# Kernel tuning notes

Hardware: AMD Instinct MI355X
Metric: run time of the kernel (lower is better)

Reference implementation:

```python
import jax, jax.numpy as jnp
import numpy as np

BANDWIDTH = 0.1
NUM_ITERS = 5


def setup_inputs() -> dict:
    key = jax.random.key(0)
    # image batch in [0,1], BCHW
    x = jax.random.uniform(key, (2, 3, 96, 96), dtype=jnp.float32)
    return {"x": x}


def reference(x):
    # Mean-shift filtering: each pixel feature y is iteratively moved to the
    # Gaussian-kernel weighted mean of ALL original pixel features:
    #   y_{t+1} = sum_j exp(-||y_t - x_j||^2 / (2 bw^2)) x_j / sum_j exp(...)
    B, C, H, W = x.shape
    N = H * W
    pts = x.reshape(B, C, N).transpose(0, 2, 1)  # [B, N, C] original points
    inv2bw2 = jnp.float32(1.0 / (2.0 * BANDWIDTH * BANDWIDTH))
    x_sq = jnp.sum(pts * pts, axis=-1)  # [B, N]

    def step(y, _):
        # squared pairwise distances via ||y||^2 + ||x||^2 - 2 y.x  -> [B, N, N]
        y_sq = jnp.sum(y * y, axis=-1)  # [B, N]
        d2 = y_sq[:, :, None] + x_sq[:, None, :] - 2.0 * jnp.einsum(
            'bnc,bmc->bnm', y, pts)
        w = jnp.exp(-jnp.maximum(d2, 0.0) * inv2bw2)  # Gaussian kernel weights
        num = jnp.einsum('bnm,bmc->bnc', w, pts)  # weighted sum of points
        den = jnp.sum(w, axis=-1, keepdims=True)  # normalizer (>= 1, self-weight)
        return num / den, None

    y, _ = jax.lax.scan(step, pts, None, length=NUM_ITERS)
    return y.transpose(0, 2, 1).reshape(B, C, H, W)
```

## Files before the change

### kernel.cpp

```cpp
#include <hip/hip_runtime.h>
#include <math.h>


#define NPTS 9216
#define NB 2
#define TOT (NB * NPTS)
#define NTIL 288
#define MSPL 6
#define MBLK 1536
#define TPW 12
#define LOG2E 1.44269504088896340736f

typedef float v2f __attribute__((ext_vector_type(2)));
typedef short bf16x8 __attribute__((ext_vector_type(8)));
typedef float f32x16 __attribute__((ext_vector_type(16)));

__device__ __forceinline__ unsigned short bf16r(float x) {
    unsigned u = __float_as_uint(x);
    return (unsigned short)((u + 0x7fffu + ((u >> 16) & 1u)) >> 16);
}
__device__ __forceinline__ float bf16f(unsigned short h) {
    return __uint_as_float((unsigned)h << 16);
}

__global__ __launch_bounds__(256) void ms_feat(const float* __restrict__ x,
                                               short* __restrict__ pfeat,
                                               float4* __restrict__ pts4,
                                               float s) {
    int gid = blockIdx.x * 256 + threadIdx.x;
    int b = gid / NPTS, m = gid - b * NPTS;
    const float* xb = x + b * 3 * NPTS;
    float p0 = xb[m] * s, p1 = xb[NPTS + m] * s, p2 = xb[2 * NPTS + m] * s;
    float np = -fmaf(p0, p0, fmaf(p1, p1, p2 * p2));
    float a0 = 2.f * p0, a1 = 2.f * p1, a2 = 2.f * p2;
    unsigned short Ah0 = bf16r(a0), Ah1 = bf16r(a1), Ah2 = bf16r(a2);
    unsigned short Al0 = bf16r(a0 - bf16f(Ah0));
    unsigned short Al1 = bf16r(a1 - bf16f(Ah1));
    unsigned short Al2 = bf16r(a2 - bf16f(Ah2));
    unsigned short Nh = bf16r(np);
    unsigned short Nl = bf16r(np - bf16f(Nh));
    uint4* dst = (uint4*)(pfeat + (size_t)gid * 16);
    dst[0] = make_uint4((unsigned)Ah0 | ((unsigned)Ah1 << 16),
                        (unsigned)Ah2 | ((unsigned)Ah0 << 16),
                        (unsigned)Ah1 | ((unsigned)Ah2 << 16),
                        (unsigned)Al0 | ((unsigned)Al1 << 16));
    dst[1] = make_uint4((unsigned)Al2 | ((unsigned)Al0 << 16),
                        (unsigned)Al1 | ((unsigned)Al2 << 16),
                        (unsigned)Nh  | ((unsigned)Nl  << 16), 0u);
    pts4[gid] = make_float4(p0, p1, p2, 1.0f);
}

__global__ __launch_bounds__(256, 4) void ms_iter(
    const float* __restrict__ x, const float4* __restrict__ accIn,
    float4* __restrict__ accOut, const short* __restrict__ pfeat,
    const float4* __restrict__ pts4, float s, int first) {

    __shared__ float4 lds4[MBLK];

    const int tid = threadIdx.x;
    const int l   = tid & 63;
    const int wv  = tid >> 6;
    const int col = l & 31;
    const int hi  = l >> 5;

    int bid = blockIdx.x;
    const int b  = bid / (MSPL * NTIL);
    int r        = bid - b * (MSPL * NTIL);
    const int nt = r / MSPL;
    const int mc = r - nt * MSPL;
    const int n  = nt * 32 + col;
    const int mbase = mc * MBLK;

    {
        const float4* src = pts4 + (size_t)b * NPTS + mbase;
        for (int i = tid; i < MBLK; i += 256) lds4[i] = src[i];
    }

    float y0, y1, y2;
    if (first) {
        const float* xb = x + b * 3 * NPTS;
        y0 = xb[n] * s; y1 = xb[NPTS + n] * s; y2 = xb[2 * NPTS + n] * s;
    } else {
        float4 a = accIn[b * NPTS + n];
        float inv = 1.0f / a.w;
        y0 = a.x * inv; y1 = a.y * inv; y2 = a.z * inv;
    }
    float ny = -fmaf(y0, y0, fmaf(y1, y1, y2 * y2));
    unsigned short Yh0 = bf16r(y0), Yh1 = bf16r(y1), Yh2 = bf16r(y2);
    unsigned short Yl0 = bf16r(y0 - bf16f(Yh0));
    unsigned short Yl1 = bf16r(y1 - bf16f(Yh1));
    unsigned short Yl2 = bf16r(y2 - bf16f(Yh2));
    union { unsigned w[4]; bf16x8 v; } yf;
    if (hi == 0) {
        yf.w[0] = (unsigned)Yh0 | ((unsigned)Yh1 << 16);
        yf.w[1] = (unsigned)Yh2 | ((unsigned)Yl0 << 16);
        yf.w[2] = (unsigned)Yl1 | ((unsigned)Yl2 << 16);
        yf.w[3] = (unsigned)Yh0 | ((unsigned)Yh1 << 16);
    } else {
        yf.w[0] = (unsigned)Yh2 | ((unsigned)Yl0 << 16);
        yf.w[1] = (unsigned)Yl1 | ((unsigned)Yl2 << 16);
        yf.w[2] = 0x3F803F80u;
        yf.w[3] = 0u;
    }

    f32x16 cin;
#pragma unroll
    for (int i = 0; i < 16; ++i) cin[i] = ny;

    v2f Axy0 = (v2f){0.f, 0.f}, Azw0 = (v2f){0.f, 0.f};
    v2f Axy1 = (v2f){0.f, 0.f}, Azw1 = (v2f){0.f, 0.f};

    const short* pfl = pfeat + (size_t)b * NPTS * 16 +
                       (size_t)(mbase + wv * TPW * 32 + col) * 16 + 8 * hi;

    __syncthreads();

    bf16x8 pf_n = *(const bf16x8*)pfl;

#pragma unroll 2
    for (int tt = 0; tt < TPW; ++tt) {
        bf16x8 pf = pf_n;
        pf_n = *(const bf16x8*)(pfl + (size_t)(tt + 1) * 512);

        const int m0L = (wv * TPW + tt) * 32;
        const float4* pb = lds4 + m0L + 4 * hi;
        float4 P[16];
#pragma unroll
        for (int q = 0; q < 4; ++q) {
            P[4 * q + 0] = pb[8 * q + 0];
            P[4 * q + 1] = pb[8 * q + 1];
            P[4 * q + 2] = pb[8 * q + 2];
            P[4 * q + 3] = pb[8 * q + 3];
        }

        f32x16 u = __builtin_amdgcn_mfma_f32_32x32x16_bf16(pf, yf.v, cin,
                                                           0, 0, 0);
#pragma unroll
        for (int q = 0; q < 4; ++q) {
            float w0 = __builtin_amdgcn_exp2f(u[4 * q + 0]);
            float w1 = __builtin_amdgcn_exp2f(u[4 * q + 1]);
            float w2 = __builtin_amdgcn_exp2f(u[4 * q + 2]);
            float w3 = __builtin_amdgcn_exp2f(u[4 * q + 3]);
            float4 P0 = P[4 * q + 0], P1 = P[4 * q + 1];
            float4 P2 = P[4 * q + 2], P3 = P[4 * q + 3];
            if (q & 1) {
                Axy1 = __builtin_elementwise_fma((v2f){w0, w0}, (v2f){P0.x, P0.y}, Axy1);
                Azw1 = __builtin_elementwise_fma((v2f){w0, w0}, (v2f){P0.z, P0.w}, Azw1);
                Axy1 = __builtin_elementwise_fma((v2f){w1, w1}, (v2f){P1.x, P1.y}, Axy1);
                Azw1 = __builtin_elementwise_fma((v2f){w1, w1}, (v2f){P1.z, P1.w}, Azw1);
                Axy1 = __builtin_elementwise_fma((v2f){w2, w2}, (v2f){P2.x, P2.y}, Axy1);
                Azw1 = __builtin_elementwise_fma((v2f){w2, w2}, (v2f){P2.z, P2.w}, Azw1);
                Axy1 = __builtin_elementwise_fma((v2f){w3, w3}, (v2f){P3.x, P3.y}, Axy1);
                Azw1 = __builtin_elementwise_fma((v2f){w3, w3}, (v2f){P3.z, P3.w}, Azw1);
            } else {
                Axy0 = __builtin_elementwise_fma((v2f){w0, w0}, (v2f){P0.x, P0.y}, Axy0);
                Azw0 = __builtin_elementwise_fma((v2f){w0, w0}, (v2f){P0.z, P0.w}, Azw0);
                Axy0 = __builtin_elementwise_fma((v2f){w1, w1}, (v2f){P1.x, P1.y}, Axy0);
                Azw0 = __builtin_elementwise_fma((v2f){w1, w1}, (v2f){P1.z, P1.w}, Azw0);
                Axy0 = __builtin_elementwise_fma((v2f){w2, w2}, (v2f){P2.x, P2.y}, Axy0);
                Azw0 = __builtin_elementwise_fma((v2f){w2, w2}, (v2f){P2.z, P2.w}, Azw0);
                Axy0 = __builtin_elementwise_fma((v2f){w3, w3}, (v2f){P3.x, P3.y}, Axy0);
                Azw0 = __builtin_elementwise_fma((v2f){w3, w3}, (v2f){P3.z, P3.w}, Azw0);
            }
        }
    }

    v2f Axy = Axy0 + Axy1;
    v2f Azw = Azw0 + Azw1;

    float hx = __shfl(Axy[0], col + 32);
    float hy = __shfl(Axy[1], col + 32);
    float hz = __shfl(Azw[0], col + 32);
    float hd = __shfl(Azw[1], col + 32);
    if (l < 32) {
        float* dst = (float*)&accOut[b * NPTS + n];
        atomicAdd(dst + 0, Axy[0] + hx);
        atomicAdd(dst + 1, Axy[1] + hy);
        atomicAdd(dst + 2, Azw[0] + hz);
        atomicAdd(dst + 3, Azw[1] + hd);
    }
}

__global__ __launch_bounds__(256) void ms_pack(const float4* __restrict__ acc4,
                                               float* __restrict__ out,
                                               float invs) {
    int gid = blockIdx.x * 256 + threadIdx.x;
    int b = gid / NPTS;
    int n = gid - b * NPTS;
    float4 a = acc4[gid];
    float f = invs / a.w;
    float* ob = out + b * 3 * NPTS;
    ob[n]            = a.x * f;
    ob[NPTS + n]     = a.y * f;
    ob[2 * NPTS + n] = a.z * f;
}

extern "C" void kernel_launch(void* const* d_in, const int* in_sizes, int n_in,
                              void* d_out, int out_size, void* d_ws, size_t ws_size,
                              hipStream_t stream) {
    const float* x = (const float*)d_in[0];
    float* out = (float*)d_out;
    float s = sqrtf(50.0f * LOG2E);

    float4* acc   = (float4*)d_ws;
    short*  pfeat = (short*)(acc + (size_t)5 * TOT);
    float4* pts4  = (float4*)(pfeat + (size_t)TOT * 16);

    hipMemsetAsync(acc, 0, (size_t)5 * TOT * sizeof(float4), stream);
    ms_feat<<<TOT / 256, 256, 0, stream>>>(x, pfeat, pts4, s);

    for (int it = 0; it < 5; ++it) {
        const float4* accIn = (it == 0) ? nullptr : acc + (size_t)(it - 1) * TOT;
        ms_iter<<<NB * NTIL * MSPL, 256, 0, stream>>>(
            x, accIn, acc + (size_t)it * TOT, pfeat, pts4, s, it == 0 ? 1 : 0);
    }
    ms_pack<<<TOT / 256, 256, 0, stream>>>(acc + (size_t)4 * TOT, out, 1.0f / s);
}
```

Baseline: 277.3 us.

## Software-pipeline MFMA one tile ahead and double-buffer LDS point loads

Restructures the inner tile loop so the MFMA for the next tile is issued before the exp2/FMA accumulation of the current tile. LDS point loads for the next quad group are double-buffered in registers, and global feature loads are prefetched two tiles ahead. The aim is to hide MFMA latency and LDS load latency behind VALU work. In exchange it raises register pressure under the 4-waves launch bound, and it pads LDS by 8 float4 to cover the final lookahead read.

```diff
diff --git a/kernel.cpp b/kernel.cpp
--- a/kernel.cpp
+++ b/kernel.cpp
@@ -50,12 +50,52 @@
     pts4[gid] = make_float4(p0, p1, p2, 1.0f);
 }
 
+#define QGRP(U, q, PU0, PU1, PU2, PU3, PL0, PL1, PL2, PL3, DG, AX, AZ)      \
+    {                                                                       \
+        PL0 = ptile[8 * (DG) + 0];                                          \
+        PL1 = ptile[8 * (DG) + 1];                                          \
+        PL2 = ptile[8 * (DG) + 2];                                          \
+        PL3 = ptile[8 * (DG) + 3];                                          \
+        float w0 = __builtin_amdgcn_exp2f(U[4 * (q) + 0]);                  \
+        float w1 = __builtin_amdgcn_exp2f(U[4 * (q) + 1]);                  \
+        float w2 = __builtin_amdgcn_exp2f(U[4 * (q) + 2]);                  \
+        float w3 = __builtin_amdgcn_exp2f(U[4 * (q) + 3]);                  \
+        AX = __builtin_elementwise_fma((v2f){w0, w0}, (v2f){PU0.x, PU0.y}, AX); \
+        AZ = __builtin_elementwise_fma((v2f){w0, w0}, (v2f){PU0.z, PU0.w}, AZ); \
+        AX = __builtin_elementwise_fma((v2f){w1, w1}, (v2f){PU1.x, PU1.y}, AX); \
+        AZ = __builtin_elementwise_fma((v2f){w1, w1}, (v2f){PU1.z, PU1.w}, AZ); \
+        AX = __builtin_elementwise_fma((v2f){w2, w2}, (v2f){PU2.x, PU2.y}, AX); \
+        AZ = __builtin_elementwise_fma((v2f){w2, w2}, (v2f){PU2.z, PU2.w}, AZ); \
+        AX = __builtin_elementwise_fma((v2f){w3, w3}, (v2f){PU3.x, PU3.y}, AX); \
+        AZ = __builtin_elementwise_fma((v2f){w3, w3}, (v2f){PU3.z, PU3.w}, AZ); \
+    }
+
+#define TBODY(CUR, NXT, PFB)                                                \
+    {                                                                       \
+        NXT = __builtin_amdgcn_mfma_f32_32x32x16_bf16(PFB, yf.v, cin, 0, 0, 0); \
+        PFB = *(const bf16x8*)(pfl + 1536);                                 \
+        QGRP(CUR, 0, PA0, PA1, PA2, PA3, PB0, PB1, PB2, PB3, 1, Axy0, Azw0) \
+        QGRP(CUR, 1, PB0, PB1, PB2, PB3, PA0, PA1, PA2, PA3, 2, Axy1, Azw1) \
+        QGRP(CUR, 2, PA0, PA1, PA2, PA3, PB0, PB1, PB2, PB3, 3, Axy0, Azw0) \
+        QGRP(CUR, 3, PB0, PB1, PB2, PB3, PA0, PA1, PA2, PA3, 4, Axy1, Azw1) \
+        pfl += 512;                                                         \
+        ptile += 32;                                                        \
+    }
+
+#define TLAST(CUR)                                                          \
+    {                                                                       \
+        QGRP(CUR, 0, PA0, PA1, PA2, PA3, PB0, PB1, PB2, PB3, 1, Axy0, Azw0) \
+        QGRP(CUR, 1, PB0, PB1, PB2, PB3, PA0, PA1, PA2, PA3, 2, Axy1, Azw1) \
+        QGRP(CUR, 2, PA0, PA1, PA2, PA3, PB0, PB1, PB2, PB3, 3, Axy0, Azw0) \
+        QGRP(CUR, 3, PB0, PB1, PB2, PB3, PA0, PA1, PA2, PA3, 4, Axy1, Azw1) \
+    }
+
 __global__ __launch_bounds__(256, 4) void ms_iter(
     const float* __restrict__ x, const float4* __restrict__ accIn,
     float4* __restrict__ accOut, const short* __restrict__ pfeat,
     const float4* __restrict__ pts4, float s, int first) {
 
-    __shared__ float4 lds4[MBLK];
+    __shared__ float4 lds4[MBLK + 8];
 
     const int tid = threadIdx.x;
     const int l   = tid & 63;
@@ -112,58 +152,26 @@
 
     const short* pfl = pfeat + (size_t)b * NPTS * 16 +
                        (size_t)(mbase + wv * TPW * 32 + col) * 16 + 8 * hi;
+    const float4* ptile = lds4 + wv * TPW * 32 + 4 * hi;
+
+    f32x16 uP, uN;
+    float4 PA0, PA1, PA2, PA3, PB0, PB1, PB2, PB3;
+
+    bf16x8 f0   = *(const bf16x8*)(pfl);
+    bf16x8 pfb1 = *(const bf16x8*)(pfl + 512);
+    bf16x8 pfb0 = *(const bf16x8*)(pfl + 1024);
 
     __syncthreads();
 
-    bf16x8 pf_n = *(const bf16x8*)pfl;
-
-#pragma unroll 2
-    for (int tt = 0; tt < TPW; ++tt) {
-        bf16x8 pf = pf_n;
-        pf_n = *(const bf16x8*)(pfl + (size_t)(tt + 1) * 512);
-
-        const int m0L = (wv * TPW + tt) * 32;
-        const float4* pb = lds4 + m0L + 4 * hi;
-        float4 P[16];
-#pragma unroll
-        for (int q = 0; q < 4; ++q) {
-            P[4 * q + 0] = pb[8 * q + 0];
-            P[4 * q + 1] = pb[8 * q + 1];
-            P[4 * q + 2] = pb[8 * q + 2];
-            P[4 * q + 3] = pb[8 * q + 3];
-        }
-
-        f32x16 u = __builtin_amdgcn_mfma_f32_32x32x16_bf16(pf, yf.v, cin,
-                                                           0, 0, 0);
-#pragma unroll
-        for (int q = 0; q < 4; ++q) {
-            float w0 = __builtin_amdgcn_exp2f(u[4 * q + 0]);
-            float w1 = __builtin_amdgcn_exp2f(u[4 * q + 1]);
-            float w2 = __builtin_amdgcn_exp2f(u[4 * q + 2]);
-            float w3 = __builtin_amdgcn_exp2f(u[4 * q + 3]);
-            float4 P0 = P[4 * q + 0], P1 = P[4 * q + 1];
-            float4 P2 = P[4 * q + 2], P3 = P[4 * q + 3];
-            if (q & 1) {
-                Axy1 = __builtin_elementwise_fma((v2f){w0, w0}, (v2f){P0.x, P0.y}, Axy1);
-                Azw1 = __builtin_elementwise_fma((v2f){w0, w0}, (v2f){P0.z, P0.w}, Azw1);
-                Axy1 = __builtin_elementwise_fma((v2f){w1, w1}, (v2f){P1.x, P1.y}, Axy1);
-                Azw1 = __builtin_elementwise_fma((v2f){w1, w1}, (v2f){P1.z, P1.w}, Azw1);
-                Axy1 = __builtin_elementwise_fma((v2f){w2, w2}, (v2f){P2.x, P2.y}, Axy1);
-                Azw1 = __builtin_elementwise_fma((v2f){w2, w2}, (v2f){P2.z, P2.w}, Azw1);
-                Axy1 = __builtin_elementwise_fma((v2f){w3, w3}, (v2f){P3.x, P3.y}, Axy1);
-                Azw1 = __builtin_elementwise_fma((v2f){w3, w3}, (v2f){P3.z, P3.w}, Azw1);
-            } else {
-                Axy0 = __builtin_elementwise_fma((v2f){w0, w0}, (v2f){P0.x, P0.y}, Axy0);
-                Azw0 = __builtin_elementwise_fma((v2f){w0, w0}, (v2f){P0.z, P0.w}, Azw0);
-                Axy0 = __builtin_elementwise_fma((v2f){w1, w1}, (v2f){P1.x, P1.y}, Axy0);
-                Azw0 = __builtin_elementwise_fma((v2f){w1, w1}, (v2f){P1.z, P1.w}, Azw0);
-                Axy0 = __builtin_elementwise_fma((v2f){w2, w2}, (v2f){P2.x, P2.y}, Axy0);
-                Azw0 = __builtin_elementwise_fma((v2f){w2, w2}, (v2f){P2.z, P2.w}, Azw0);
-                Axy0 = __builtin_elementwise_fma((v2f){w3, w3}, (v2f){P3.x, P3.y}, Axy0);
-                Azw0 = __builtin_elementwise_fma((v2f){w3, w3}, (v2f){P3.z, P3.w}, Azw0);
-            }
-        }
-    }
+    uP = __builtin_amdgcn_mfma_f32_32x32x16_bf16(f0, yf.v, cin, 0, 0, 0);
+    PA0 = ptile[0]; PA1 = ptile[1]; PA2 = ptile[2]; PA3 = ptile[3];
+
+    for (int t2 = 0; t2 < TPW - 2; t2 += 2) {
+        TBODY(uP, uN, pfb1)
+        TBODY(uN, uP, pfb0)
+    }
+    TBODY(uP, uN, pfb1)
+    TLAST(uN)
 
     v2f Axy = Axy0 + Axy1;
     v2f Azw = Azw0 + Azw1;
```

After: 386.3 us. 1.39x slower.

## Compute weighted point sums with bf16 MFMA instead of scalar FMAs

Applied to the files above, without the earlier changes.

The second matmul (kernel weights times points) moves from per-lane scalar FMA accumulation over LDS-staged float4 points to MFMA. The exp2 weights are rounded to bf16 and packed with perm, and points are stored as a channel-major hi/lo bf16 split in a new feature buffer. The LDS staging and block barrier are removed, and the loop is restructured into a two-deep software pipeline over distance MFMAs. Occupancy hint drops from 4 to 3 waves per SIMD. Weight rounding to bf16 adds error to the numerator and denominator sums.

```diff
diff --git a/kernel.cpp b/kernel.cpp
--- a/kernel.cpp
+++ b/kernel.cpp
@@ -11,9 +11,10 @@
 #define TPW 12
 #define LOG2E 1.44269504088896340736f
 
-typedef float v2f __attribute__((ext_vector_type(2)));
+typedef short bf16x4 __attribute__((ext_vector_type(4)));
 typedef short bf16x8 __attribute__((ext_vector_type(8)));
 typedef float f32x16 __attribute__((ext_vector_type(16)));
+typedef union { bf16x4 q[4]; bf16x8 h[2]; } vfrag;
 
 __device__ __forceinline__ unsigned short bf16r(float x) {
     unsigned u = __float_as_uint(x);
@@ -25,7 +26,7 @@
 
 __global__ __launch_bounds__(256) void ms_feat(const float* __restrict__ x,
                                                short* __restrict__ pfeat,
-                                               float4* __restrict__ pts4,
+                                               short* __restrict__ vfeat,
                                                float s) {
     int gid = blockIdx.x * 256 + threadIdx.x;
     int b = gid / NPTS, m = gid - b * NPTS;
@@ -47,15 +48,64 @@
     dst[1] = make_uint4((unsigned)Al2 | ((unsigned)Al0 << 16),
                         (unsigned)Al1 | ((unsigned)Al2 << 16),
                         (unsigned)Nh  | ((unsigned)Nl  << 16), 0u);
-    pts4[gid] = make_float4(p0, p1, p2, 1.0f);
-}
-
-__global__ __launch_bounds__(256, 4) void ms_iter(
+    unsigned short Vh0 = bf16r(p0), Vh1 = bf16r(p1), Vh2 = bf16r(p2);
+    unsigned short Vl0 = bf16r(p0 - bf16f(Vh0));
+    unsigned short Vl1 = bf16r(p1 - bf16f(Vh1));
+    unsigned short Vl2 = bf16r(p2 - bf16f(Vh2));
+    short* vb = vfeat + (size_t)b * 8 * NPTS + m;
+    vb[0]        = (short)Vh0;
+    vb[NPTS]     = (short)Vh1;
+    vb[2 * NPTS] = (short)Vh2;
+    vb[3 * NPTS] = (short)0x3F80;
+    vb[4 * NPTS] = (short)Vl0;
+    vb[5 * NPTS] = (short)Vl1;
+    vb[6 * NPTS] = (short)Vl2;
+    vb[7 * NPTS] = 0;
+}
+
+#define VLOAD(VD, P)                                                        \
+    {                                                                       \
+        VD.q[0] = *(const bf16x4*)(P);                                      \
+        VD.q[1] = *(const bf16x4*)((P) + 8);                                \
+        VD.q[2] = *(const bf16x4*)((P) + 16);                               \
+        VD.q[3] = *(const bf16x4*)((P) + 24);                               \
+    }
+
+#define PROC(U, VD)                                                         \
+    {                                                                       \
+        unsigned t0  = __float_as_uint(__builtin_amdgcn_exp2f(U[0]))  + 0x8000u; \
+        unsigned t1  = __float_as_uint(__builtin_amdgcn_exp2f(U[1]))  + 0x8000u; \
+        unsigned t2  = __float_as_uint(__builtin_amdgcn_exp2f(U[2]))  + 0x8000u; \
+        unsigned t3  = __float_as_uint(__builtin_amdgcn_exp2f(U[3]))  + 0x8000u; \
+        unsigned t4  = __float_as_uint(__builtin_amdgcn_exp2f(U[4]))  + 0x8000u; \
+        unsigned t5  = __float_as_uint(__builtin_amdgcn_exp2f(U[5]))  + 0x8000u; \
+        unsigned t6  = __float_as_uint(__builtin_amdgcn_exp2f(U[6]))  + 0x8000u; \
+        unsigned t7  = __float_as_uint(__builtin_amdgcn_exp2f(U[7]))  + 0x8000u; \
+        unsigned t8  = __float_as_uint(__builtin_amdgcn_exp2f(U[8]))  + 0x8000u; \
+        unsigned t9  = __float_as_uint(__builtin_amdgcn_exp2f(U[9]))  + 0x8000u; \
+        unsigned t10 = __float_as_uint(__builtin_amdgcn_exp2f(U[10])) + 0x8000u; \
+        unsigned t11 = __float_as_uint(__builtin_amdgcn_exp2f(U[11])) + 0x8000u; \
+        unsigned t12 = __float_as_uint(__builtin_amdgcn_exp2f(U[12])) + 0x8000u; \
+        unsigned t13 = __float_as_uint(__builtin_amdgcn_exp2f(U[13])) + 0x8000u; \
+        unsigned t14 = __float_as_uint(__builtin_amdgcn_exp2f(U[14])) + 0x8000u; \
+        unsigned t15 = __float_as_uint(__builtin_amdgcn_exp2f(U[15])) + 0x8000u; \
+        union { unsigned w[4]; bf16x8 v; } F0, F1;                          \
+        F0.w[0] = __builtin_amdgcn_perm(t1,  t0,  0x07060302u);             \
+        F0.w[1] = __builtin_amdgcn_perm(t3,  t2,  0x07060302u);             \
+        F0.w[2] = __builtin_amdgcn_perm(t5,  t4,  0x07060302u);             \
+        F0.w[3] = __builtin_amdgcn_perm(t7,  t6,  0x07060302u);             \
+        F1.w[0] = __builtin_amdgcn_perm(t9,  t8,  0x07060302u);             \
+        F1.w[1] = __builtin_amdgcn_perm(t11, t10, 0x07060302u);             \
+        F1.w[2] = __builtin_amdgcn_perm(t13, t12, 0x07060302u);             \
+        F1.w[3] = __builtin_amdgcn_perm(t15, t14, 0x07060302u);             \
+        po = __builtin_amdgcn_mfma_f32_32x32x16_bf16(VD.h[0], F0.v, po, 0, 0, 0); \
+        po = __builtin_amdgcn_mfma_f32_32x32x16_bf16(VD.h[1], F1.v, po, 0, 0, 0); \
+    }
+
+__global__ __launch_bounds__(256, 3) void ms_iter(
     const float* __restrict__ x, const float4* __restrict__ accIn,
     float4* __restrict__ accOut, const short* __restrict__ pfeat,
-    const float4* __restrict__ pts4, float s, int first) {
-
-    __shared__ float4 lds4[MBLK];
+    const short* __restrict__ vfeat, float s, int first) {
 
     const int tid = threadIdx.x;
     const int l   = tid & 63;
@@ -70,11 +120,6 @@
     const int mc = r - nt * MSPL;
     const int n  = nt * 32 + col;
     const int mbase = mc * MBLK;
-
-    {
-        const float4* src = pts4 + (size_t)b * NPTS + mbase;
-        for (int i = tid; i < MBLK; i += 256) lds4[i] = src[i];
-    }
 
     float y0, y1, y2;
     if (first) {
@@ -103,81 +148,51 @@
         yf.w[3] = 0u;
     }
 
-    f32x16 cin;
+    f32x16 cin, po;
 #pragma unroll
     for (int i = 0; i < 16; ++i) cin[i] = ny;
-
-    v2f Axy0 = (v2f){0.f, 0.f}, Azw0 = (v2f){0.f, 0.f};
-    v2f Axy1 = (v2f){0.f, 0.f}, Azw1 = (v2f){0.f, 0.f};
+#pragma unroll
+    for (int i = 0; i < 16; ++i) po[i] = 0.f;
 
     const short* pfl = pfeat + (size_t)b * NPTS * 16 +
                        (size_t)(mbase + wv * TPW * 32 + col) * 16 + 8 * hi;
-
-    __syncthreads();
-
-    bf16x8 pf_n = *(const bf16x8*)pfl;
-
-#pragma unroll 2
-    for (int tt = 0; tt < TPW; ++tt) {
-        bf16x8 pf = pf_n;
-        pf_n = *(const bf16x8*)(pfl + (size_t)(tt + 1) * 512);
-
-        const int m0L = (wv * TPW + tt) * 32;
-        const float4* pb = lds4 + m0L + 4 * hi;
-        float4 P[16];
-#pragma unroll
-        for (int q = 0; q < 4; ++q) {
-            P[4 * q + 0] = pb[8 * q + 0];
-            P[4 * q + 1] = pb[8 * q + 1];
-            P[4 * q + 2] = pb[8 * q + 2];
-            P[4 * q + 3] = pb[8 * q + 3];
-        }
-
-        f32x16 u = __builtin_amdgcn_mfma_f32_32x32x16_bf16(pf, yf.v, cin,
-                                                           0, 0, 0);
-#pragma unroll
-        for (int q = 0; q < 4; ++q) {
-            float w0 = __builtin_amdgcn_exp2f(u[4 * q + 0]);
-            float w1 = __builtin_amdgcn_exp2f(u[4 * q + 1]);
-            float w2 = __builtin_amdgcn_exp2f(u[4 * q + 2]);
-            float w3 = __builtin_amdgcn_exp2f(u[4 * q + 3]);
-            float4 P0 = P[4 * q + 0], P1 = P[4 * q + 1];
-            float4 P2 = P[4 * q + 2], P3 = P[4 * q + 3];
-            if (q & 1) {
-                Axy1 = __builtin_elementwise_fma((v2f){w0, w0}, (v2f){P0.x, P0.y}, Axy1);
-                Azw1 = __builtin_elementwise_fma((v2f){w0, w0}, (v2f){P0.z, P0.w}, Azw1);
-                Axy1 = __builtin_elementwise_fma((v2f){w1, w1}, (v2f){P1.x, P1.y}, Axy1);
-                Azw1 = __builtin_elementwise_fma((v2f){w1, w1}, (v2f){P1.z, P1.w}, Azw1);
-                Axy1 = __builtin_elementwise_fma((v2f){w2, w2}, (v2f){P2.x, P2.y}, Axy1);
-                Azw1 = __builtin_elementwise_fma((v2f){w2, w2}, (v2f){P2.z, P2.w}, Azw1);
-                Axy1 = __builtin_elementwise_fma((v2f){w3, w3}, (v2f){P3.x, P3.y}, Axy1);
-                Azw1 = __builtin_elementwise_fma((v2f){w3, w3}, (v2f){P3.z, P3.w}, Azw1);
-            } else {
-                Axy0 = __builtin_elementwise_fma((v2f){w0, w0}, (v2f){P0.x, P0.y}, Axy0);
-                Azw0 = __builtin_elementwise_fma((v2f){w0, w0}, (v2f){P0.z, P0.w}, Azw0);
-                Axy0 = __builtin_elementwise_fma((v2f){w1, w1}, (v2f){P1.x, P1.y}, Axy0);
-                Azw0 = __builtin_elementwise_fma((v2f){w1, w1}, (v2f){P1.z, P1.w}, Azw0);
-                Axy0 = __builtin_elementwise_fma((v2f){w2, w2}, (v2f){P2.x, P2.y}, Axy0);
-                Azw0 = __builtin_elementwise_fma((v2f){w2, w2}, (v2f){P2.z, P2.w}, Azw0);
-                Axy0 = __builtin_elementwise_fma((v2f){w3, w3}, (v2f){P3.x, P3.y}, Axy0);
-                Azw0 = __builtin_elementwise_fma((v2f){w3, w3}, (v2f){P3.z, P3.w}, Azw0);
-            }
-        }
-    }
-
-    v2f Axy = Axy0 + Axy1;
-    v2f Azw = Azw0 + Azw1;
-
-    float hx = __shfl(Axy[0], col + 32);
-    float hy = __shfl(Axy[1], col + 32);
-    float hz = __shfl(Azw[0], col + 32);
-    float hd = __shfl(Azw[1], col + 32);
+    const int cmin = col < 8 ? col : 7;
+    const short* vp = vfeat + (size_t)b * 8 * NPTS + (size_t)cmin * NPTS +
+                      (mbase + wv * TPW * 32) + 4 * hi;
+
+    bf16x8 pfA = *(const bf16x8*)(pfl);
+    bf16x8 pfB = *(const bf16x8*)(pfl + 512);
+    vfrag VA, VB;
+    VLOAD(VA, vp)
+    VLOAD(VB, vp + 32)
+    f32x16 uA = __builtin_amdgcn_mfma_f32_32x32x16_bf16(pfA, yf.v, cin, 0, 0, 0);
+    f32x16 uB;
+
+    for (int i = 0; i < (TPW - 2) / 2; ++i) {
+        uB = __builtin_amdgcn_mfma_f32_32x32x16_bf16(pfB, yf.v, cin, 0, 0, 0);
+        pfA = *(const bf16x8*)(pfl + 1024);
+        PROC(uA, VA)
+        VLOAD(VA, vp + 64)
+        pfl += 512; vp += 32;
+        uA = __builtin_amdgcn_mfma_f32_32x32x16_bf16(pfA, yf.v, cin, 0, 0, 0);
+        pfB = *(const bf16x8*)(pfl + 1024);
+        PROC(uB, VB)
+        VLOAD(VB, vp + 64)
+        pfl += 512; vp += 32;
+    }
+    uB = __builtin_amdgcn_mfma_f32_32x32x16_bf16(pfB, yf.v, cin, 0, 0, 0);
+    PROC(uA, VA)
+    PROC(uB, VB)
+
+    float lx = __shfl(po[0], col + 32);
+    float ly = __shfl(po[1], col + 32);
+    float lz = __shfl(po[2], col + 32);
     if (l < 32) {
         float* dst = (float*)&accOut[b * NPTS + n];
-        atomicAdd(dst + 0, Axy[0] + hx);
-        atomicAdd(dst + 1, Axy[1] + hy);
-        atomicAdd(dst + 2, Azw[0] + hz);
-        atomicAdd(dst + 3, Azw[1] + hd);
+        atomicAdd(dst + 0, po[0] + lx);
+        atomicAdd(dst + 1, po[1] + ly);
+        atomicAdd(dst + 2, po[2] + lz);
+        atomicAdd(dst + 3, po[3]);
     }
 }
 
@@ -204,15 +219,15 @@
 
     float4* acc   = (float4*)d_ws;
     short*  pfeat = (short*)(acc + (size_t)5 * TOT);
-    float4* pts4  = (float4*)(pfeat + (size_t)TOT * 16);
+    short*  vfeat = pfeat + (size_t)TOT * 16;
 
     hipMemsetAsync(acc, 0, (size_t)5 * TOT * sizeof(float4), stream);
-    ms_feat<<<TOT / 256, 256, 0, stream>>>(x, pfeat, pts4, s);
+    ms_feat<<<TOT / 256, 256, 0, stream>>>(x, pfeat, vfeat, s);
 
     for (int it = 0; it < 5; ++it) {
         const float4* accIn = (it == 0) ? nullptr : acc + (size_t)(it - 1) * TOT;
         ms_iter<<<NB * NTIL * MSPL, 256, 0, stream>>>(
-            x, accIn, acc + (size_t)it * TOT, pfeat, pts4, s, it == 0 ? 1 : 0);
+            x, accIn, acc + (size_t)it * TOT, pfeat, vfeat, s, it == 0 ? 1 : 0);
     }
     ms_pack<<<TOT / 256, 256, 0, stream>>>(acc + (size_t)4 * TOT, out, 1.0f / s);
 }
```

Result: no change. 282.2 us (+1.8%).
